# Kernel optimization log

Measured on AMD Instinct MI355X. Metric: run time of the kernel, lower is better.

The kernel has to match this reference:

```python
import jax, jax.numpy as jnp
import numpy as np

B, T, F = 32, 1024, 512
EPS = 1e-6


def setup_inputs() -> dict:
    key = jax.random.key(0)
    k1, k2, k3 = jax.random.split(key, 3)
    x = jax.random.normal(k1, (B, T, F), dtype=jnp.float32)
    aggr_w = jax.random.normal(k2, (F, 1), dtype=jnp.float32) / np.sqrt(F).astype(np.float32)
    aggr_b = jnp.zeros((1,), dtype=jnp.float32)
    seq_len = jax.random.randint(k3, (B,), T // 2, T + 1, dtype=jnp.int32).at[0].set(T)
    return {"x": x, "aggr_w": aggr_w, "aggr_b": aggr_b, "seq_len": seq_len}


def reference(x, aggr_w, aggr_b, seq_len):
    # --- gate weights: sigmoid(Linear(F->1)) ---
    w = jax.nn.sigmoid(jnp.einsum('btf,fo->bto', x, aggr_w) + aggr_b)  # [B,T,1]
    ws = w[..., 0]                                                      # [B,T]

    # --- valley detection (comparisons on detached neighbors; non-diff anyway) ---
    wd = jax.lax.stop_gradient(ws)
    sb = jnp.pad(wd[:, :-1], ((0, 0), (1, 0)))  # previous frame, 0 at t=0
    sa = jnp.pad(wd[:, 1:], ((0, 0), (0, 1)))   # next frame, 0 at t=T-1
    valley = (wd < sb) & (wd < sa)              # [B,T] bool

    start_mask = valley.at[:, 0].set(True)
    end_mask = valley.at[:, 0].set(False).at[:, -1].set(True)
    counts = jnp.sum(start_mask, axis=1)        # segments per batch (== end count)

    # sorted valley positions per batch (pad value T pushes pads to the end)
    idx = jnp.arange(T, dtype=jnp.int32)
    starts = jnp.sort(jnp.where(start_mask, idx, T), axis=1)            # [B,T]
    ends = jnp.minimum(jnp.sort(jnp.where(end_mask, idx, T), axis=1) + 2, T)

    # statically pad max_counts -> T; torch zero-fills unused segment rows
    seg_ids = jnp.arange(T, dtype=jnp.int32)
    valid = seg_ids[None, :] < counts[:, None]                          # [B,S]
    seg_start = jnp.where(valid, starts, 0)
    seg_end = jnp.where(valid, ends, 0)

    # segment indicator == utri[end] - utri[start]  (1 for start <= t < end)
    t = jnp.arange(T, dtype=jnp.int32)
    seg_mask = ((t[None, None, :] >= seg_start[:, :, None]) &
                (t[None, None, :] < seg_end[:, :, None])).astype(x.dtype)  # [B,S,T]

    # segment-weighted mean (dense bmm like torch)
    alpha_h = ws[..., None] * x                                         # [B,T,F]
    num = jnp.einsum('bst,btf->bsf', seg_mask, alpha_h)                 # [B,S,F]
    den = jnp.maximum(jnp.einsum('bst,bt->bs', seg_mask, ws), EPS)      # [B,S]
    out = num / den[..., None]                                          # [B,S,F]

    # new sequence mask (torch uses dynamic x.shape[1] == max(counts))
    lengths = seq_len.astype(jnp.float32)
    max_counts = jnp.max(counts).astype(jnp.float32)
    new_lengths = (lengths / lengths[0] * max_counts).astype(jnp.int32)  # [B]
    new_mask = seg_ids[None, :] < new_lengths[:, None]                   # [B,S]
    return out, new_mask
```

## Files before the change

kernel.cpp:

```cpp
#include <hip/hip_runtime.h>

#define TT 1024
#define FF 512
#define BB 32
#define MAXSEG 513

__global__ __launch_bounds__(256) void gate_kernel(const float* __restrict__ x,
                                                   const float* __restrict__ w,
                                                   const float* __restrict__ bias,
                                                   float* __restrict__ ws) {
    int wid  = threadIdx.x >> 6;
    int lane = threadIdx.x & 63;
    int row  = blockIdx.x * 4 + wid;
    const float4* xr = (const float4*)(x + (size_t)row * FF);
    const float4* wr = (const float4*)w;
    float4 x0 = xr[lane * 2],     x1 = xr[lane * 2 + 1];
    float4 w0 = wr[lane * 2],     w1 = wr[lane * 2 + 1];
    double acc = (double)x0.x * w0.x + (double)x0.y * w0.y +
                 (double)x0.z * w0.z + (double)x0.w * w0.w +
                 (double)x1.x * w1.x + (double)x1.y * w1.y +
                 (double)x1.z * w1.z + (double)x1.w * w1.w;
    #pragma unroll
    for (int off = 32; off; off >>= 1) acc += __shfl_down(acc, off);
    if (lane == 0) {
        float z = (float)acc + bias[0];
        ws[row] = 1.0f / (1.0f + expf(-z));
    }
}

__global__ __launch_bounds__(1024) void seg_kernel(const float* __restrict__ ws,
                                                   int* __restrict__ seg_start,
                                                   int* __restrict__ seg_end,
                                                   float* __restrict__ den,
                                                   int* __restrict__ counts) {
    int b = blockIdx.x, t = threadIdx.x;
    __shared__ float w[TT];
    __shared__ float p[TT];
    __shared__ unsigned long long words[16];
    __shared__ float wavesum[16];
    __shared__ int sst[MAXSEG];
    __shared__ int sen[MAXSEG];

    w[t] = ws[b * TT + t];
    __syncthreads();

    float wt = w[t];
    bool valley = (t > 0) && (t < TT - 1) && (wt < w[t - 1]) && (wt < w[t + 1]);
    unsigned long long m = __ballot(valley);
    int wid = t >> 6, lane = t & 63;
    if (lane == 0) words[wid] = m;

    float s = wt;
    #pragma unroll
    for (int off = 1; off < 64; off <<= 1) {
        float v = __shfl_up(s, off);
        if (lane >= off) s += v;
    }
    if (lane == 63) wavesum[wid] = s;
    __syncthreads();

    float offset = 0.0f;
    for (int i = 0; i < wid; ++i) offset += wavesum[i];
    p[t] = s + offset;

    int before = __popcll(m & ((1ull << lane) - 1ull));
    int total = 0;
    for (int i = 0; i < 16; ++i) {
        int pc = __popcll(words[i]);
        if (i < wid) before += pc;
        total += pc;
    }
    if (valley) {
        int en = t + 2; if (en > TT) en = TT;
        sst[before + 1] = t;
        sen[before]     = en;
    }
    if (t == 0) {
        sst[0]     = 0;
        sen[total] = TT;
        counts[b]  = total + 1;
    }
    __syncthreads();

    int cnt = total + 1;
    if (t < cnt) {
        int st = sst[t], en = sen[t];
        seg_start[b * TT + t] = st;
        seg_end  [b * TT + t] = en;
        float d = p[en - 1] - (st > 0 ? p[st - 1] : 0.0f);
        den[b * TT + t] = fmaxf(d, 1e-6f);
    }
}

__global__ __launch_bounds__(128) void out_kernel(const float* __restrict__ x,
                                                  const float* __restrict__ ws,
                                                  const int* __restrict__ seg_start,
                                                  const int* __restrict__ seg_end,
                                                  const float* __restrict__ den,
                                                  const int* __restrict__ counts,
                                                  float* __restrict__ out) {
    int bs = blockIdx.x;
    int b  = bs >> 10;
    int s  = bs & 1023;
    int f  = threadIdx.x * 4;
    float4* o = (float4*)(out + (size_t)bs * FF + f);
    if (s >= counts[b]) {
        *o = make_float4(0.f, 0.f, 0.f, 0.f);
        return;
    }
    int st = seg_start[bs], en = seg_end[bs];
    float d = den[bs];
    const float* xb = x + (size_t)b * TT * FF;
    float4 acc = make_float4(0.f, 0.f, 0.f, 0.f);
    for (int t = st; t < en; ++t) {
        float wt = ws[b * TT + t];
        float4 xv = *(const float4*)(xb + (size_t)t * FF + f);
        acc.x += wt * xv.x; acc.y += wt * xv.y;
        acc.z += wt * xv.z; acc.w += wt * xv.w;
    }
    *o = make_float4(acc.x / d, acc.y / d, acc.z / d, acc.w / d);
}

__global__ __launch_bounds__(1024) void mask_kernel(const int* __restrict__ counts,
                                                    const int* __restrict__ seq_len,
                                                    float* __restrict__ mask) {
    int b = blockIdx.x, s = threadIdx.x;
    int maxc = 0;
    #pragma unroll
    for (int i = 0; i < BB; ++i) maxc = max(maxc, counts[i]);
    float l0 = (float)seq_len[0];
    float v  = ((float)seq_len[b] / l0) * (float)maxc;
    int nl = (int)v;
    mask[b * TT + s] = (s < nl) ? 1.0f : 0.0f;
}

extern "C" void kernel_launch(void* const* d_in, const int* in_sizes, int n_in,
                              void* d_out, int out_size, void* d_ws, size_t ws_size,
                              hipStream_t stream) {
    const float* x    = (const float*)d_in[0];
    const float* aw   = (const float*)d_in[1];
    const float* ab   = (const float*)d_in[2];
    const int*   seq  = (const int*)d_in[3];
    float* out = (float*)d_out;

    float* ws     = (float*)d_ws;
    float* den    = ws + BB * TT;
    int*   sstart = (int*)(ws + 2 * BB * TT);
    int*   send   = (int*)(ws + 3 * BB * TT);
    int*   counts = (int*)(ws + 4 * BB * TT);

    gate_kernel<<<BB * TT / 4, 256, 0, stream>>>(x, aw, ab, ws);
    seg_kernel<<<BB, 1024, 0, stream>>>(ws, sstart, send, den, counts);
    out_kernel<<<BB * TT, 128, 0, stream>>>(x, ws, sstart, send, den, counts, out);
    mask_kernel<<<BB, 1024, 0, stream>>>(counts, seq, out + (size_t)BB * TT * FF);
}
```

Before: 46.43 us.

## Fuse mask kernel into out_kernel, use wave-per-segment and nontemporal stores

Moves the mask computation into the first block of each batch in out_kernel, which removes one kernel launch. Restructures out_kernel so each 64-lane wave handles one segment row with 8 floats per lane, and unrolls the time loop by two with split accumulators. Output is written with nontemporal stores to reduce cache pollution, and the per-element divide becomes a multiply by a reciprocal. This risks small rounding differences and adds work to some blocks.

New measurement: 44.44 us. 4.3% less time.

```diff
diff --git a/kernel.cpp b/kernel.cpp
--- a/kernel.cpp
+++ b/kernel.cpp
@@ -4,6 +4,12 @@
 #define FF 512
 #define BB 32
 #define MAXSEG 513
+
+typedef float f32x4 __attribute__((ext_vector_type(4)));
+
+__device__ __forceinline__ void nt_store4(float* p, f32x4 v) {
+    __builtin_nontemporal_store(v, (f32x4*)p);
+}
 
 __global__ __launch_bounds__(256) void gate_kernel(const float* __restrict__ x,
                                                    const float* __restrict__ w,
@@ -92,46 +98,67 @@
     }
 }
 
-__global__ __launch_bounds__(128) void out_kernel(const float* __restrict__ x,
+__global__ __launch_bounds__(256) void out_kernel(const float* __restrict__ x,
                                                   const float* __restrict__ ws,
                                                   const int* __restrict__ seg_start,
                                                   const int* __restrict__ seg_end,
                                                   const float* __restrict__ den,
                                                   const int* __restrict__ counts,
+                                                  const int* __restrict__ seq,
                                                   float* __restrict__ out) {
-    int bs = blockIdx.x;
+    if ((blockIdx.x & 255) == 0) {
+        int bb = blockIdx.x >> 8;
+        int maxc = 0;
+        #pragma unroll
+        for (int i = 0; i < BB; ++i) maxc = max(maxc, counts[i]);
+        float l0 = (float)seq[0];
+        float v  = ((float)seq[bb] / l0) * (float)maxc;
+        int nl = (int)v;
+        float* mrow = out + (size_t)BB * TT * FF + (size_t)bb * TT;
+        int s4 = threadIdx.x * 4;
+        f32x4 mv;
+        mv.x = (s4 + 0 < nl) ? 1.0f : 0.0f;
+        mv.y = (s4 + 1 < nl) ? 1.0f : 0.0f;
+        mv.z = (s4 + 2 < nl) ? 1.0f : 0.0f;
+        mv.w = (s4 + 3 < nl) ? 1.0f : 0.0f;
+        nt_store4(mrow + s4, mv);
+    }
+
+    int wid  = threadIdx.x >> 6;
+    int lane = threadIdx.x & 63;
+    int bs = blockIdx.x * 4 + wid;
     int b  = bs >> 10;
     int s  = bs & 1023;
-    int f  = threadIdx.x * 4;
-    float4* o = (float4*)(out + (size_t)bs * FF + f);
+    float* orow = out + (size_t)bs * FF + lane * 8;
     if (s >= counts[b]) {
-        *o = make_float4(0.f, 0.f, 0.f, 0.f);
+        f32x4 z = 0.0f;
+        nt_store4(orow, z);
+        nt_store4(orow + 4, z);
         return;
     }
     int st = seg_start[bs], en = seg_end[bs];
-    float d = den[bs];
-    const float* xb = x + (size_t)b * TT * FF;
-    float4 acc = make_float4(0.f, 0.f, 0.f, 0.f);
-    for (int t = st; t < en; ++t) {
-        float wt = ws[b * TT + t];
-        float4 xv = *(const float4*)(xb + (size_t)t * FF + f);
-        acc.x += wt * xv.x; acc.y += wt * xv.y;
-        acc.z += wt * xv.z; acc.w += wt * xv.w;
+    float inv = 1.0f / den[bs];
+    const f32x4* xb = (const f32x4*)(x + (size_t)b * TT * FF) + lane * 2;
+    const float* wsr = ws + b * TT;
+    f32x4 a0 = 0.0f, a1 = 0.0f, c0 = 0.0f, c1 = 0.0f;
+    int t = st;
+    for (; t + 2 <= en; t += 2) {
+        float w0 = wsr[t], w1 = wsr[t + 1];
+        f32x4 p0 = xb[(size_t)t * (FF / 4)];
+        f32x4 p1 = xb[(size_t)t * (FF / 4) + 1];
+        f32x4 q0 = xb[(size_t)(t + 1) * (FF / 4)];
+        f32x4 q1 = xb[(size_t)(t + 1) * (FF / 4) + 1];
+        a0 += w0 * p0; a1 += w0 * p1;
+        c0 += w1 * q0; c1 += w1 * q1;
     }
-    *o = make_float4(acc.x / d, acc.y / d, acc.z / d, acc.w / d);
-}
-
-__global__ __launch_bounds__(1024) void mask_kernel(const int* __restrict__ counts,
-                                                    const int* __restrict__ seq_len,
-                                                    float* __restrict__ mask) {
-    int b = blockIdx.x, s = threadIdx.x;
-    int maxc = 0;
-    #pragma unroll
-    for (int i = 0; i < BB; ++i) maxc = max(maxc, counts[i]);
-    float l0 = (float)seq_len[0];
-    float v  = ((float)seq_len[b] / l0) * (float)maxc;
-    int nl = (int)v;
-    mask[b * TT + s] = (s < nl) ? 1.0f : 0.0f;
+    if (t < en) {
+        float w0 = wsr[t];
+        a0 += w0 * xb[(size_t)t * (FF / 4)];
+        a1 += w0 * xb[(size_t)t * (FF / 4) + 1];
+    }
+    a0 += c0; a1 += c1;
+    nt_store4(orow,     a0 * inv);
+    nt_store4(orow + 4, a1 * inv);
 }
 
 extern "C" void kernel_launch(void* const* d_in, const int* in_sizes, int n_in,
@@ -151,6 +178,6 @@
 
     gate_kernel<<<BB * TT / 4, 256, 0, stream>>>(x, aw, ab, ws);
     seg_kernel<<<BB, 1024, 0, stream>>>(ws, sstart, send, den, counts);
-    out_kernel<<<BB * TT, 128, 0, stream>>>(x, ws, sstart, send, den, counts, out);
-    mask_kernel<<<BB, 1024, 0, stream>>>(counts, seq, out + (size_t)BB * TT * FF);
+    out_kernel<<<BB * TT / 4, 256, 0, stream>>>(x, ws, sstart, send, den, counts,
+                                                seq, out);
 }
```
